# Kernel tuning notes

Measured on AMD Instinct MI355X. Metric: run time of the kernel, lower is better.

The kernel has to match this reference:

```python
import jax, jax.numpy as jnp
import numpy as np

D = 2048
H = 16
HD = D // H  # 128


def setup_inputs() -> dict:
    key = jax.random.key(0)
    k1, k2, k3 = jax.random.split(key, 3)
    x = jax.random.normal(k1, (2, 2048, D), dtype=jnp.float32)
    # nn.Linear(d, 3d, bias=False): weight [3d, d]; y = x @ W.T
    w_qkv = jax.random.normal(k2, (3 * D, D), dtype=jnp.float32) * (1.0 / np.sqrt(D))
    w_o = jax.random.normal(k3, (D, D), dtype=jnp.float32) * (1.0 / np.sqrt(D))
    return {"x": x, "w_qkv": w_qkv, "w_o": w_o}


def reference(x, w_qkv, w_o):
    B, T, _ = x.shape
    qkv = jnp.einsum('btd,ed->bte', x, w_qkv)  # [B,T,3D]
    q, k, v = jnp.split(qkv, 3, axis=-1)
    # [B,T,D] -> [B,H,T,hd]
    q = q.reshape(B, T, H, HD).transpose(0, 2, 1, 3)
    k = k.reshape(B, T, H, HD).transpose(0, 2, 1, 3)
    v = v.reshape(B, T, H, HD).transpose(0, 2, 1, 3)
    att = jnp.einsum('bhtd,bhsd->bhts', q, k) / np.sqrt(HD).astype(np.float32)
    att = jax.nn.softmax(att, axis=-1)
    y = jnp.einsum('bhts,bhsd->bhtd', att, v)
    y = y.transpose(0, 2, 1, 3).reshape(B, T, D)
    return jnp.einsum('btd,ed->bte', y, w_o)
```

## Files before the change

### kernel.cpp

```cpp
#include <hip/hip_runtime.h>
#include <hip/hip_bf16.h>
#include <math.h>

typedef __bf16 bf16_t;
typedef __attribute__((ext_vector_type(8))) __bf16 bx8;
typedef __attribute__((ext_vector_type(4))) __bf16 bx4;
typedef __attribute__((ext_vector_type(4))) float fx4;

#define DEV __device__ __forceinline__

DEV void async_copy16(void* lds, const void* g) {
    __builtin_amdgcn_global_load_lds(
        (const __attribute__((address_space(1))) unsigned int*)g,
        (__attribute__((address_space(3))) unsigned int*)lds, 16, 0, 0);
}

__global__ void __launch_bounds__(256) cvt_bf16(const float* __restrict__ in,
                                                bf16_t* __restrict__ out, int n) {
    int i = (blockIdx.x * 256 + threadIdx.x) * 4;
    if (i + 3 < n) {
        float4 v = *(const float4*)(in + i);
        bx4 o = { (__bf16)v.x, (__bf16)v.y, (__bf16)v.z, (__bf16)v.w };
        *(bx4*)(out + i) = o;
    }
}

template <bool BF16_OUT>
__global__ void __launch_bounds__(256, 2) gemm_bt(const bf16_t* __restrict__ A,
                                                  const bf16_t* __restrict__ B,
                                                  void* __restrict__ C,
                                                  int M, int N, int K) {
    __shared__ bf16_t As[128 * 32];
    __shared__ bf16_t Bs[128 * 32];
    const int tid = threadIdx.x;
    const int w = tid >> 6, lane = tid & 63;
    const int ln = lane & 15, quad = lane >> 4;
    const int m0 = blockIdx.y * 128, n0 = blockIdx.x * 128;
    const int wm = (w >> 1) * 64, wn = (w & 1) * 64;

    fx4 acc[4][4];
#pragma unroll
    for (int i = 0; i < 4; ++i)
#pragma unroll
        for (int j = 0; j < 4; ++j) acc[i][j] = (fx4){0.f, 0.f, 0.f, 0.f};

    for (int k0 = 0; k0 < K; k0 += 32) {
#pragma unroll
        for (int call = 0; call < 2; ++call) {
            int c = w * 128 + call * 64 + lane;
            int row = c >> 2, kc = c & 3;
            async_copy16(As + (size_t)(w * 128 + call * 64) * 8,
                         A + (size_t)(m0 + row) * K + k0 + kc * 8);
            async_copy16(Bs + (size_t)(w * 128 + call * 64) * 8,
                         B + (size_t)(n0 + row) * K + k0 + kc * 8);
        }
        __syncthreads();

        bx8 af[4], bf[4];
#pragma unroll
        for (int i = 0; i < 4; ++i)
            af[i] = *(const bx8*)(As + (size_t)(wm + i * 16 + ln) * 32 + quad * 8);
#pragma unroll
        for (int j = 0; j < 4; ++j)
            bf[j] = *(const bx8*)(Bs + (size_t)(wn + j * 16 + ln) * 32 + quad * 8);
#pragma unroll
        for (int i = 0; i < 4; ++i)
#pragma unroll
            for (int j = 0; j < 4; ++j)
                acc[i][j] = __builtin_amdgcn_mfma_f32_16x16x32_bf16(af[i], bf[j], acc[i][j], 0, 0, 0);
        __syncthreads();
    }

#pragma unroll
    for (int i = 0; i < 4; ++i) {
        int mrow = m0 + wm + i * 16 + quad * 4;
#pragma unroll
        for (int j = 0; j < 4; ++j) {
            int ncol = n0 + wn + j * 16 + ln;
#pragma unroll
            for (int r = 0; r < 4; ++r) {
                if (BF16_OUT)
                    ((bf16_t*)C)[(size_t)(mrow + r) * N + ncol] = (__bf16)acc[i][j][r];
                else
                    ((float*)C)[(size_t)(mrow + r) * N + ncol] = acc[i][j][r];
            }
        }
    }
}

__global__ void __launch_bounds__(256) vtrans(const bf16_t* __restrict__ qkv,
                                              bf16_t* __restrict__ vt) {
    __shared__ bf16_t tile[64][65];
    const int tid = threadIdx.x;
    const int bh = blockIdx.z;
    const int b = bh >> 4, h = bh & 15;
    const int t0 = blockIdx.x * 64, hd0 = blockIdx.y * 64;
    const bf16_t* src = qkv + (size_t)(b * 2048 + t0) * 6144 + 4096 + h * 128 + hd0;
    const int rr = tid >> 6, cc = tid & 63;
#pragma unroll
    for (int i = 0; i < 16; ++i)
        tile[rr + i * 4][cc] = src[(size_t)(rr + i * 4) * 6144 + cc];
    __syncthreads();
    bf16_t* dst = vt + ((size_t)bh * 128 + hd0) * 2048 + t0;
#pragma unroll
    for (int i = 0; i < 16; ++i)
        dst[(size_t)(rr + i * 4) * 2048 + cc] = tile[cc][rr + i * 4];
}

__global__ void __launch_bounds__(256, 2) attn(const bf16_t* __restrict__ qkv,
                                               const bf16_t* __restrict__ vt,
                                               bf16_t* __restrict__ y) {
    __shared__ bf16_t Ks[128 * 128];
    __shared__ bf16_t Vs[128 * 128];
    const int tid = threadIdx.x;
    const int w = tid >> 6, lane = tid & 63;
    const int ln = lane & 15, quad = lane >> 4;
    const int lin = blockIdx.x;
    const int slot = lin >> 3;
    const int bh = (lin & 7) + ((slot >> 4) << 3);
    const int qt = slot & 15;
    const int b = bh >> 4, h = bh & 15;
    const float CEXP = 0.08838834764831845f * 1.44269504088896340f;

    const bf16_t* Qb = qkv + (size_t)(b * 2048 + qt * 128) * 6144 + h * 128;
    const bf16_t* Kb = qkv + (size_t)(b * 2048) * 6144 + 2048 + h * 128;
    const bf16_t* Vb = vt + (size_t)bh * 128 * 2048;

    bx8 qf[2][4];
#pragma unroll
    for (int i = 0; i < 2; ++i)
#pragma unroll
        for (int kk = 0; kk < 4; ++kk)
            qf[i][kk] = *(const bx8*)(Qb + (size_t)(w * 32 + i * 16 + ln) * 6144 + kk * 32 + quad * 8);

    const __bf16 one = (__bf16)1.0f;
    const bx8 ones = { one, one, one, one, one, one, one, one };

    fx4 o[2][8];
#pragma unroll
    for (int i = 0; i < 2; ++i)
#pragma unroll
        for (int j = 0; j < 8; ++j) o[i][j] = (fx4){0.f, 0.f, 0.f, 0.f};
    fx4 lsum[2];
#pragma unroll
    for (int i = 0; i < 2; ++i) lsum[i] = (fx4){0.f, 0.f, 0.f, 0.f};

    for (int kt = 0; kt < 16; ++kt) {
#pragma unroll
        for (int call = 0; call < 8; ++call) {
            int cp = call * 64 + lane;
            int row = cp >> 2, piece = cp & 3;
            async_copy16(Ks + (size_t)w * 4096 + call * 512,
                         Kb + (size_t)(kt * 128 + row) * 6144 + w * 32 + piece * 8);
            async_copy16(Vs + (size_t)w * 4096 + call * 512,
                         Vb + (size_t)row * 2048 + kt * 128 + w * 32 + piece * 8);
        }
        __syncthreads();

        fx4 s[2][8];
#pragma unroll
        for (int i = 0; i < 2; ++i)
#pragma unroll
            for (int j = 0; j < 8; ++j) s[i][j] = (fx4){0.f, 0.f, 0.f, 0.f};
#pragma unroll
        for (int kk = 0; kk < 4; ++kk) {
            bx8 kf[8];
#pragma unroll
            for (int j = 0; j < 8; ++j)
                kf[j] = *(const bx8*)(Ks + (size_t)kk * 4096 + (j * 16 + ln) * 32 + quad * 8);
#pragma unroll
            for (int i = 0; i < 2; ++i)
#pragma unroll
                for (int j = 0; j < 8; ++j)
                    s[i][j] = __builtin_amdgcn_mfma_f32_16x16x32_bf16(qf[i][kk], kf[j], s[i][j], 0, 0, 0);
        }

#pragma unroll
        for (int i = 0; i < 2; ++i)
#pragma unroll
            for (int j = 0; j < 8; ++j)
#pragma unroll
                for (int r = 0; r < 4; ++r)
                    s[i][j][r] = exp2f(s[i][j][r] * CEXP);

        __syncthreads();

        bf16_t* Pw = Ks + (size_t)w * 4096;
#pragma unroll
        for (int i = 0; i < 2; ++i)
#pragma unroll
            for (int j = 0; j < 8; ++j)
#pragma unroll
                for (int r = 0; r < 4; ++r) {
                    int prow = i * 16 + quad * 4 + r;
                    Pw[(j >> 1) * 1024 + prow * 32 + (((j & 1) * 16 + ln) ^ (quad << 3))] =
                        (__bf16)s[i][j][r];
                }

#pragma unroll
        for (int kk = 0; kk < 4; ++kk) {
            bx8 pf[2], vf[8];
#pragma unroll
            for (int i = 0; i < 2; ++i)
                pf[i] = *(const bx8*)(Pw + (size_t)kk * 1024 + (i * 16 + ln) * 32 +
                                      ((quad ^ ((ln >> 2) & 3)) << 3));
#pragma unroll
            for (int j = 0; j < 8; ++j)
                vf[j] = *(const bx8*)(Vs + (size_t)kk * 4096 + (j * 16 + ln) * 32 + quad * 8);
#pragma unroll
            for (int i = 0; i < 2; ++i) {
#pragma unroll
                for (int j = 0; j < 8; ++j)
                    o[i][j] = __builtin_amdgcn_mfma_f32_16x16x32_bf16(pf[i], vf[j], o[i][j], 0, 0, 0);
                lsum[i] = __builtin_amdgcn_mfma_f32_16x16x32_bf16(pf[i], ones, lsum[i], 0, 0, 0);
            }
        }
        __syncthreads();
    }

#pragma unroll
    for (int i = 0; i < 2; ++i)
#pragma unroll
        for (int r = 0; r < 4; ++r) {
            float rl = 1.0f / lsum[i][r];
#pragma unroll
            for (int j = 0; j < 8; ++j) {
                int t = qt * 128 + w * 32 + i * 16 + quad * 4 + r;
                int col = h * 128 + j * 16 + ln;
                y[(size_t)(b * 2048 + t) * 2048 + col] = (__bf16)(o[i][j][r] * rl);
            }
        }
}

extern "C" void kernel_launch(void* const* d_in, const int* in_sizes, int n_in,
                              void* d_out, int out_size, void* d_ws, size_t ws_size,
                              hipStream_t stream) {
    const float* x    = (const float*)d_in[0];
    const float* wqkv = (const float*)d_in[1];
    const float* wo   = (const float*)d_in[2];
    float* out = (float*)d_out;
    char* ws = (char*)d_ws;

    bf16_t* Xb  = (bf16_t*)(ws);
    bf16_t* Wqb = (bf16_t*)(ws + (size_t)(16u << 20));
    bf16_t* Wob = (bf16_t*)(ws + (size_t)(40u << 20));
    bf16_t* QKV = (bf16_t*)(ws + (size_t)(48u << 20));
    bf16_t* VT  = (bf16_t*)(ws + (size_t)(96u << 20));
    bf16_t* Y   = Xb;

    cvt_bf16<<<8388608 / 1024, 256, 0, stream>>>(x, Xb, 8388608);
    cvt_bf16<<<12582912 / 1024, 256, 0, stream>>>(wqkv, Wqb, 12582912);
    cvt_bf16<<<4194304 / 1024, 256, 0, stream>>>(wo, Wob, 4194304);

    gemm_bt<true><<<dim3(48, 32), 256, 0, stream>>>(Xb, Wqb, QKV, 4096, 6144, 2048);
    vtrans<<<dim3(32, 2, 32), 256, 0, stream>>>(QKV, VT);
    attn<<<dim3(512), 256, 0, stream>>>(QKV, VT, Y);
    gemm_bt<false><<<dim3(16, 32), 256, 0, stream>>>(Y, Wob, out, 4096, 2048, 2048);
}
```

Measured before the change: 402.1 us.

## Use 256x256 double-buffered async-LDS GEMM kernel for QKV projection

Adds a new 512-thread GEMM kernel with 256x256 output tiles, a double-buffered LDS pipeline fed by global_load_lds async copies, explicit vmcnt waits, and MFMA priority hints. The QKV projection switches from the 128-tile gemm_bt to this kernel. The aim is more data reuse per tile and overlap of global loads with MFMA work. In exchange the grid shrinks to 384 blocks, one per CU at 128 KB of LDS, so occupancy is low and there is a wave-quantization risk on a 256-CU device.

```diff
diff --git a/kernel.cpp b/kernel.cpp
--- a/kernel.cpp
+++ b/kernel.cpp
@@ -84,6 +84,94 @@
                 else
                     ((float*)C)[(size_t)(mrow + r) * N + ncol] = acc[i][j][r];
             }
+        }
+    }
+}
+
+__global__ void __launch_bounds__(512, 1) gemm256_bt(const bf16_t* __restrict__ A,
+                                                     const bf16_t* __restrict__ B,
+                                                     bf16_t* __restrict__ C,
+                                                     int M, int N, int K) {
+    __shared__ bf16_t As[2 * 16384];
+    __shared__ bf16_t Bs[2 * 16384];
+    const int tid = threadIdx.x;
+    const int w = tid >> 6, lane = tid & 63;
+    const int ln = lane & 15, quad = lane >> 4;
+    const int m0 = blockIdx.y * 256, n0 = blockIdx.x * 256;
+    const int wm = (w >> 2) * 128;
+    const int wn = (w & 3) * 64;
+
+    fx4 acc[8][4];
+#pragma unroll
+    for (int i = 0; i < 8; ++i)
+#pragma unroll
+        for (int j = 0; j < 4; ++j) acc[i][j] = (fx4){0.f, 0.f, 0.f, 0.f};
+
+    const int srow = (lane >> 2);
+    const int spiece = lane & 3;
+
+#define G_STAGE(buf_, kt_)                                                              \
+    {                                                                                   \
+        _Pragma("unroll") for (int c = 0; c < 4; ++c) {                                 \
+            int R = w * 4 + c;                                                          \
+            int kplane = R >> 4;                                                        \
+            int row = ((R & 15) << 4) + srow;                                           \
+            async_copy16(As + (size_t)(buf_) * 16384 + R * 512,                         \
+                         A + (size_t)(m0 + row) * K + (kt_) * 64 + kplane * 32 + spiece * 8); \
+            async_copy16(Bs + (size_t)(buf_) * 16384 + R * 512,                         \
+                         B + (size_t)(n0 + row) * K + (kt_) * 64 + kplane * 32 + spiece * 8); \
+        }                                                                               \
+    }
+
+    const int nt = K >> 6;
+    G_STAGE(0, 0);
+
+    for (int t = 0; t < nt; ++t) {
+        const int cur = t & 1;
+        if (t + 1 < nt) {
+            G_STAGE(cur ^ 1, t + 1);
+            asm volatile("s_waitcnt vmcnt(8)" ::: "memory");
+        } else {
+            asm volatile("s_waitcnt vmcnt(0)" ::: "memory");
+        }
+        __builtin_amdgcn_sched_barrier(0);
+        __builtin_amdgcn_s_barrier();
+        __builtin_amdgcn_sched_barrier(0);
+
+        const bf16_t* Ab = As + (size_t)cur * 16384;
+        const bf16_t* Bb = Bs + (size_t)cur * 16384;
+#pragma unroll
+        for (int kk = 0; kk < 2; ++kk) {
+            bx8 af[8], bfr[4];
+#pragma unroll
+            for (int i = 0; i < 8; ++i)
+                af[i] = *(const bx8*)(Ab + (size_t)kk * 8192 + (wm + i * 16 + ln) * 32 + quad * 8);
+#pragma unroll
+            for (int j = 0; j < 4; ++j)
+                bfr[j] = *(const bx8*)(Bb + (size_t)kk * 8192 + (wn + j * 16 + ln) * 32 + quad * 8);
+            __builtin_amdgcn_s_setprio(1);
+#pragma unroll
+            for (int i = 0; i < 8; ++i)
+#pragma unroll
+                for (int j = 0; j < 4; ++j)
+                    acc[i][j] = __builtin_amdgcn_mfma_f32_16x16x32_bf16(af[i], bfr[j], acc[i][j], 0, 0, 0);
+            __builtin_amdgcn_s_setprio(0);
+        }
+        __builtin_amdgcn_sched_barrier(0);
+        __builtin_amdgcn_s_barrier();
+        __builtin_amdgcn_sched_barrier(0);
+    }
+#undef G_STAGE
+
+#pragma unroll
+    for (int i = 0; i < 8; ++i) {
+        int mrow = m0 + wm + i * 16 + quad * 4;
+#pragma unroll
+        for (int j = 0; j < 4; ++j) {
+            int ncol = n0 + wn + j * 16 + ln;
+#pragma unroll
+            for (int r = 0; r < 4; ++r)
+                C[(size_t)(mrow + r) * N + ncol] = (__bf16)acc[i][j][r];
         }
     }
 }
@@ -252,7 +340,7 @@
     cvt_bf16<<<12582912 / 1024, 256, 0, stream>>>(wqkv, Wqb, 12582912);
     cvt_bf16<<<4194304 / 1024, 256, 0, stream>>>(wo, Wob, 4194304);
 
-    gemm_bt<true><<<dim3(48, 32), 256, 0, stream>>>(Xb, Wqb, QKV, 4096, 6144, 2048);
+    gemm256_bt<<<dim3(24, 16), 512, 0, stream>>>(Xb, Wqb, QKV, 4096, 6144, 2048);
     vtrans<<<dim3(32, 2, 32), 256, 0, stream>>>(QKV, VT);
     attn<<<dim3(512), 256, 0, stream>>>(QKV, VT, Y);
     gemm_bt<false><<<dim3(16, 32), 256, 0, stream>>>(Y, Wob, out, 4096, 2048, 2048);
```

New measurement: 432.9 us. +7.7%, slower.

## Prefetch next K/V tiles asynchronously and give P its own LDS buffer

Applied to the files above, without the earlier changes.

Splits K and V staging into separate async copies. The next tile's K load is issued right after QK^T and the next V load right after PV, so global loads overlap compute. P gets a dedicated shared buffer instead of reusing the K tile, and __syncthreads is replaced by explicit vmcnt/lgkmcnt waits plus s_barrier. The extra 32KB of LDS raises per-block shared memory and may cut resident blocks per CU.

```diff
diff --git a/kernel.cpp b/kernel.cpp
--- a/kernel.cpp
+++ b/kernel.cpp
@@ -112,6 +112,7 @@
                                                bf16_t* __restrict__ y) {
     __shared__ bf16_t Ks[128 * 128];
     __shared__ bf16_t Vs[128 * 128];
+    __shared__ bf16_t Ps[4 * 4096];
     const int tid = threadIdx.x;
     const int w = tid >> 6, lane = tid & 63;
     const int ln = lane & 15, quad = lane >> 4;
@@ -145,17 +146,33 @@
 #pragma unroll
     for (int i = 0; i < 2; ++i) lsum[i] = (fx4){0.f, 0.f, 0.f, 0.f};
 
+#define STAGE_K(kt_)                                                                     \
+    {                                                                                    \
+        _Pragma("unroll") for (int call = 0; call < 8; ++call) {                         \
+            int cp = call * 64 + lane;                                                   \
+            int row = cp >> 2, piece = cp & 3;                                           \
+            async_copy16(Ks + (size_t)w * 4096 + call * 512,                             \
+                         Kb + (size_t)((kt_) * 128 + row) * 6144 + w * 32 + piece * 8);  \
+        }                                                                                \
+    }
+#define STAGE_V(kt_)                                                                     \
+    {                                                                                    \
+        _Pragma("unroll") for (int call = 0; call < 8; ++call) {                         \
+            int cp = call * 64 + lane;                                                   \
+            int row = cp >> 2, piece = cp & 3;                                           \
+            async_copy16(Vs + (size_t)w * 4096 + call * 512,                             \
+                         Vb + (size_t)row * 2048 + (kt_) * 128 + piece * 8 + w * 32);    \
+        }                                                                                \
+    }
+
+    STAGE_K(0);
+    STAGE_V(0);
+
     for (int kt = 0; kt < 16; ++kt) {
-#pragma unroll
-        for (int call = 0; call < 8; ++call) {
-            int cp = call * 64 + lane;
-            int row = cp >> 2, piece = cp & 3;
-            async_copy16(Ks + (size_t)w * 4096 + call * 512,
-                         Kb + (size_t)(kt * 128 + row) * 6144 + w * 32 + piece * 8);
-            async_copy16(Vs + (size_t)w * 4096 + call * 512,
-                         Vb + (size_t)row * 2048 + kt * 128 + w * 32 + piece * 8);
-        }
-        __syncthreads();
+        asm volatile("s_waitcnt vmcnt(8)" ::: "memory");
+        __builtin_amdgcn_sched_barrier(0);
+        __builtin_amdgcn_s_barrier();
+        __builtin_amdgcn_sched_barrier(0);
 
         fx4 s[2][8];
 #pragma unroll
@@ -174,6 +191,11 @@
                 for (int j = 0; j < 8; ++j)
                     s[i][j] = __builtin_amdgcn_mfma_f32_16x16x32_bf16(qf[i][kk], kf[j], s[i][j], 0, 0, 0);
         }
+        asm volatile("s_waitcnt lgkmcnt(0)" ::: "memory");
+        __builtin_amdgcn_sched_barrier(0);
+        __builtin_amdgcn_s_barrier();
+        __builtin_amdgcn_sched_barrier(0);
+        if (kt < 15) STAGE_K(kt + 1);
 
 #pragma unroll
         for (int i = 0; i < 2; ++i)
@@ -183,9 +205,7 @@
                 for (int r = 0; r < 4; ++r)
                     s[i][j][r] = exp2f(s[i][j][r] * CEXP);
 
-        __syncthreads();
-
-        bf16_t* Pw = Ks + (size_t)w * 4096;
+        bf16_t* Pw = Ps + (size_t)w * 4096;
 #pragma unroll
         for (int i = 0; i < 2; ++i)
 #pragma unroll
@@ -197,6 +217,12 @@
                         (__bf16)s[i][j][r];
                 }
 
+        if (kt < 15) asm volatile("s_waitcnt vmcnt(8)" ::: "memory");
+        else         asm volatile("s_waitcnt vmcnt(0)" ::: "memory");
+        __builtin_amdgcn_sched_barrier(0);
+        __builtin_amdgcn_s_barrier();
+        __builtin_amdgcn_sched_barrier(0);
+
 #pragma unroll
         for (int kk = 0; kk < 4; ++kk) {
             bx8 pf[2], vf[8];
@@ -215,8 +241,14 @@
                 lsum[i] = __builtin_amdgcn_mfma_f32_16x16x32_bf16(pf[i], ones, lsum[i], 0, 0, 0);
             }
         }
-        __syncthreads();
-    }
+        asm volatile("s_waitcnt lgkmcnt(0)" ::: "memory");
+        __builtin_amdgcn_sched_barrier(0);
+        __builtin_amdgcn_s_barrier();
+        __builtin_amdgcn_sched_barrier(0);
+        if (kt < 15) STAGE_V(kt + 1);
+    }
+#undef STAGE_K
+#undef STAGE_V
 
 #pragma unroll
     for (int i = 0; i < 2; ++i)
```

After: 440.4 us. 9.5% more time.

## Interleave QK and PV per 32-key chunk with dedicated P buffer

Applied to the files above, without the earlier changes.

Restructures the attention inner loop so each 32-key slice computes scores, exponentiates, writes P to a new small per-warp LDS buffer and immediately accumulates into O, instead of computing the full 128-key score tile first. This cuts live score registers (from 64 to 16 floats) and removes the mid-tile barrier that was needed to reuse the K buffer for P. In exchange it adds 8KB of LDS per block, which may affect the 2-blocks-per-CU occupancy target, and it adds per-chunk LDS write/read round trips with less MFMA batching.

```diff
diff --git a/kernel.cpp b/kernel.cpp
--- a/kernel.cpp
+++ b/kernel.cpp
@@ -112,6 +112,7 @@
                                                bf16_t* __restrict__ y) {
     __shared__ bf16_t Ks[128 * 128];
     __shared__ bf16_t Vs[128 * 128];
+    __shared__ bf16_t Ps[4 * 1024];
     const int tid = threadIdx.x;
     const int w = tid >> 6, lane = tid & 63;
     const int ln = lane & 15, quad = lane >> 4;
@@ -145,6 +146,8 @@
 #pragma unroll
     for (int i = 0; i < 2; ++i) lsum[i] = (fx4){0.f, 0.f, 0.f, 0.f};
 
+    bf16_t* Pw = Ps + (size_t)w * 1024;
+
     for (int kt = 0; kt < 16; ++kt) {
 #pragma unroll
         for (int call = 0; call < 8; ++call) {
@@ -157,62 +160,45 @@
         }
         __syncthreads();
 
-        fx4 s[2][8];
-#pragma unroll
-        for (int i = 0; i < 2; ++i)
-#pragma unroll
-            for (int j = 0; j < 8; ++j) s[i][j] = (fx4){0.f, 0.f, 0.f, 0.f};
-#pragma unroll
-        for (int kk = 0; kk < 4; ++kk) {
-            bx8 kf[8];
-#pragma unroll
-            for (int j = 0; j < 8; ++j)
-                kf[j] = *(const bx8*)(Ks + (size_t)kk * 4096 + (j * 16 + ln) * 32 + quad * 8);
+#pragma unroll
+        for (int q = 0; q < 4; ++q) {
+            fx4 s[2][2];
 #pragma unroll
             for (int i = 0; i < 2; ++i)
 #pragma unroll
-                for (int j = 0; j < 8; ++j)
-                    s[i][j] = __builtin_amdgcn_mfma_f32_16x16x32_bf16(qf[i][kk], kf[j], s[i][j], 0, 0, 0);
-        }
-
-#pragma unroll
-        for (int i = 0; i < 2; ++i)
-#pragma unroll
-            for (int j = 0; j < 8; ++j)
-#pragma unroll
-                for (int r = 0; r < 4; ++r)
-                    s[i][j][r] = exp2f(s[i][j][r] * CEXP);
-
-        __syncthreads();
-
-        bf16_t* Pw = Ks + (size_t)w * 4096;
-#pragma unroll
-        for (int i = 0; i < 2; ++i)
-#pragma unroll
-            for (int j = 0; j < 8; ++j)
-#pragma unroll
-                for (int r = 0; r < 4; ++r) {
-                    int prow = i * 16 + quad * 4 + r;
-                    Pw[(j >> 1) * 1024 + prow * 32 + (((j & 1) * 16 + ln) ^ (quad << 3))] =
-                        (__bf16)s[i][j][r];
+                for (int jj = 0; jj < 2; ++jj) s[i][jj] = (fx4){0.f, 0.f, 0.f, 0.f};
+#pragma unroll
+            for (int kk = 0; kk < 4; ++kk) {
+                bx8 kf0 = *(const bx8*)(Ks + (size_t)kk * 4096 + ((2 * q) * 16 + ln) * 32 + quad * 8);
+                bx8 kf1 = *(const bx8*)(Ks + (size_t)kk * 4096 + ((2 * q + 1) * 16 + ln) * 32 + quad * 8);
+#pragma unroll
+                for (int i = 0; i < 2; ++i) {
+                    s[i][0] = __builtin_amdgcn_mfma_f32_16x16x32_bf16(qf[i][kk], kf0, s[i][0], 0, 0, 0);
+                    s[i][1] = __builtin_amdgcn_mfma_f32_16x16x32_bf16(qf[i][kk], kf1, s[i][1], 0, 0, 0);
                 }
-
-#pragma unroll
-        for (int kk = 0; kk < 4; ++kk) {
-            bx8 pf[2], vf[8];
+            }
+
 #pragma unroll
             for (int i = 0; i < 2; ++i)
-                pf[i] = *(const bx8*)(Pw + (size_t)kk * 1024 + (i * 16 + ln) * 32 +
-                                      ((quad ^ ((ln >> 2) & 3)) << 3));
-#pragma unroll
-            for (int j = 0; j < 8; ++j)
-                vf[j] = *(const bx8*)(Vs + (size_t)kk * 4096 + (j * 16 + ln) * 32 + quad * 8);
+#pragma unroll
+                for (int jj = 0; jj < 2; ++jj)
+#pragma unroll
+                    for (int r = 0; r < 4; ++r) {
+                        float p = exp2f(s[i][jj][r] * CEXP);
+                        int prow = i * 16 + quad * 4 + r;
+                        Pw[prow * 32 + ((jj * 16 + ln) ^ (quad << 3))] = (__bf16)p;
+                    }
+
 #pragma unroll
             for (int i = 0; i < 2; ++i) {
-#pragma unroll
-                for (int j = 0; j < 8; ++j)
-                    o[i][j] = __builtin_amdgcn_mfma_f32_16x16x32_bf16(pf[i], vf[j], o[i][j], 0, 0, 0);
-                lsum[i] = __builtin_amdgcn_mfma_f32_16x16x32_bf16(pf[i], ones, lsum[i], 0, 0, 0);
+                bx8 pf = *(const bx8*)(Pw + (size_t)(i * 16 + ln) * 32 +
+                                       ((quad ^ ((ln >> 2) & 3)) << 3));
+#pragma unroll
+                for (int j = 0; j < 8; ++j) {
+                    bx8 vf = *(const bx8*)(Vs + (size_t)q * 4096 + (j * 16 + ln) * 32 + quad * 8);
+                    o[i][j] = __builtin_amdgcn_mfma_f32_16x16x32_bf16(pf, vf, o[i][j], 0, 0, 0);
+                }
+                lsum[i] = __builtin_amdgcn_mfma_f32_16x16x32_bf16(pf, ones, lsum[i], 0, 0, 0);
             }
         }
         __syncthreads();
```

Measured after the change: 401.5 us. No clear change (-0.2%).
